# Kernel tuning notes

Hardware: AMD Instinct MI355X
Metric: run time of the kernel (lower is better)

The kernel has to match this reference:

```python
import jax, jax.numpy as jnp
import numpy as np

D, NH, K, FF, S, B = 256, 4, 1024, 1024, 2048, 4  # nhead*d_model must equal key_feature_dim=1024


def _ln(x, g, b, eps=1e-5):
    m = jnp.mean(x, axis=-1, keepdims=True)
    v = jnp.mean((x - m) ** 2, axis=-1, keepdims=True)
    return (x - m) / jnp.sqrt(v + eps) * g + b


def _l2norm(x, eps=1e-12):  # F.normalize(p=2, dim=-1)
    n = jnp.sqrt(jnp.sum(x * x, axis=-1, keepdims=True))
    return x / jnp.maximum(n, eps)


def setup_inputs() -> dict:
    key = jax.random.key(0)
    ks = jax.random.split(key, 16)
    def rn(i, shape, s):
        return jax.random.normal(ks[i], shape, jnp.float32) * jnp.float32(s)
    z = lambda shape: jnp.zeros(shape, jnp.float32)
    o = lambda shape: jnp.ones(shape, jnp.float32)
    return {
        "srcc": jax.random.normal(ks[0], (S, B, D), jnp.float32),
        "memory": jax.random.normal(ks[1], (S, B, D), jnp.float32),
        # per-head RelationUnit weights (stacked over NH heads)
        "WK": rn(2, (NH, K, D), np.sqrt(2.0 / K)),
        "WQ": rn(3, (NH, K, D), np.sqrt(2.0 / K)),
        "WV": rn(4, (NH, D, D), np.sqrt(2.0 / D)),
        "Wt": rn(5, (NH, D, D), np.sqrt(1.0 / D)),   # trans_conv
        # per-head TransNonlinear (extra_nonlinear)
        "e1w": rn(6, (NH, K, D), np.sqrt(1.0 / D)), "e1b": z((NH, K)),
        "e2w": rn(7, (NH, D, K), np.sqrt(1.0 / K)), "e2b": z((NH, D)),
        "eg": o((NH, D)), "eb": z((NH, D)),
        "Wout": rn(8, (D, NH * D), np.sqrt(1.0 / (NH * D))),  # trans_conv_out
        # decoder-layer FFN + norms
        "l1w": rn(9, (FF, D), np.sqrt(1.0 / D)), "l1b": z((FF,)),
        "l2w": rn(10, (D, FF), np.sqrt(1.0 / FF)), "l2b": z((D,)),
        "n1g": o((D,)), "n1b": z((D,)),
        "n3g": o((D,)), "n3b": z((D,)),
    }


def _forward(srcc, memory, WK, WQ, WV, Wt, e1w, e1b, e2w, e2b, eg, eb,
             Wout, l1w, l1b, l2w, l2b, n1g, n1b, n3g, n3b):
    # RMA(query=memory, key=srcc, value=srcc); dropout = identity (eval mode)
    q, kv = memory, srcc  # [S,B,D]
    wk = _l2norm(jnp.einsum('sbd,hkd->hsbk', kv, WK))   # [h,S,B,K]
    wq = _l2norm(jnp.einsum('sbd,hkd->hsbk', q, WQ))
    dot = jnp.einsum('hqbk,hsbk->hbqs', wq, wk)          # [h,B,Sq,Sk]
    aff = jax.nn.softmax(dot, axis=-1)
    # custom renormalization over the *query* axis (torch dim=1 of [B,Sq,Sk])
    aff = aff / (1e-9 + jnp.sum(aff, axis=2, keepdims=True))
    wv = jnp.einsum('sbd,hed->hbse', kv, WV)             # [h,B,Sk,D]
    o = jnp.einsum('hbqs,hbse->hqbe', aff, wv)           # [h,Sq,B,D]
    ru = jax.nn.relu(jnp.einsum('hqbd,hed->hqbe', q[None] - o, Wt))
    # per-head TransNonlinear
    hmid = jax.nn.relu(jnp.einsum('hqbd,hkd->hqbk', ru, e1w) + e1b[:, None, None, :])
    s2 = jnp.einsum('hqbk,hdk->hqbd', hmid, e2w) + e2b[:, None, None, :]
    xh = _ln(ru + s2, eg[:, None, None, :], eb[:, None, None, :])  # [h,S,B,D]
    cat = jnp.moveaxis(xh, 0, 2).reshape(q.shape[0], q.shape[1], NH * D)  # concat heads
    rma_out = jnp.einsum('sbk,dk->sbd', cat, Wout)       # [S,B,D]
    # decoder layer: note the faithful `[0]` indexing from the source
    srcc2 = rma_out[0]                                    # [B,D]
    x = _ln(memory + srcc2[None, :, :], n1g, n1b)         # broadcast residual
    ff = jax.nn.relu(x @ l1w.T + l1b) @ l2w.T + l2b
    return _ln(x + ff, n3g, n3b)


def reference(srcc, memory, WK, WQ, WV, Wt, e1w, e1b, e2w, e2b, eg, eb,
              Wout, l1w, l1b, l2w, l2b, n1g, n1b, n3g, n3b):
    return _forward(srcc, memory, WK, WQ, WV, Wt, e1w, e1b, e2w, e2b, eg, eb,
                    Wout, l1w, l1b, l2w, l2b, n1g, n1b, n3g, n3b)
```

## Files before the change

kernel.cpp:

```cpp
#include <hip/hip_runtime.h>
#include <stdint.h>
#include <stdio.h>

#define S_  2048
#define B_  4
#define D_  256
#define NH_ 4
#define K_  1024
#define FF_ 1024
#define M_  (S_*B_)
#define HB_ (NH_*B_)
#define HBH_ (HB_/2)

#define LDSROW 136

typedef float  f32x4  __attribute__((ext_vector_type(4)));
typedef __bf16 bf16x8 __attribute__((ext_vector_type(8)));

__device__ __forceinline__ float bf2f(unsigned short u) {
  union { unsigned int i; float f; } v; v.i = ((unsigned int)u) << 16; return v.f;
}
__device__ __forceinline__ unsigned short f2bf(float f) {
  union { float f; unsigned int i; } v; v.f = f;
  unsigned int r = v.i + 0x7fffu + ((v.i >> 16) & 1u);
  return (unsigned short)(r >> 16);
}

__device__ __forceinline__ void gld_lds16(const void* g, void* l) {
  __builtin_amdgcn_global_load_lds(
      (__attribute__((address_space(1))) void*)(uintptr_t)g,
      (__attribute__((address_space(3))) void*)(uintptr_t)l, 16, 0, 0);
}

__device__ __forceinline__ void gemm_kloop(
    const unsigned short* __restrict__ Ag, const unsigned short* __restrict__ Bg,
    int lda, int ldb, int kdim,
    unsigned short* __restrict__ smA, unsigned short* __restrict__ smB,
    f32x4 acc[4][4])
{
  const int t    = threadIdx.x;
  const int wave = t >> 6;
  const int lane = t & 63;
  const int wm   = (wave >> 1) << 6;
  const int wn   = (wave & 1) << 6;
  const int c16  = lane & 15;
  const int quad = lane >> 4;

  for (int kc = 0; kc < kdim; kc += 64) {
    __syncthreads();
#pragma unroll
    for (int it = 0; it < 4; ++it) {
      int c   = it*256 + t;
      int row = c >> 3;
      int g   = (c & 7) ^ (row & 7);
      const unsigned short* ga = Ag + (size_t)row*lda + kc + g*8;
      const unsigned short* gb = Bg + (size_t)row*ldb + kc + g*8;
      unsigned short* la = smA + (size_t)(it*256 + wave*64)*8;
      unsigned short* lb = smB + (size_t)(it*256 + wave*64)*8;
      gld_lds16(ga, la);
      gld_lds16(gb, lb);
    }
    asm volatile("s_waitcnt vmcnt(0)" ::: "memory");
    __syncthreads();
#pragma unroll
    for (int ks = 0; ks < 2; ++ks) {
      bf16x8 av[4], bv[4];
#pragma unroll
      for (int i = 0; i < 4; ++i) {
        int ra = wm + i*16 + c16;
        av[i] = *(const bf16x8*)(smA + ra*64 + (((ks*4 + quad) ^ (ra & 7)))*8);
        int rb = wn + i*16 + c16;
        bv[i] = *(const bf16x8*)(smB + rb*64 + (((ks*4 + quad) ^ (rb & 7)))*8);
      }
#pragma unroll
      for (int i = 0; i < 4; ++i)
#pragma unroll
        for (int j = 0; j < 4; ++j)
          acc[i][j] = __builtin_amdgcn_mfma_f32_16x16x32_bf16(av[i], bv[j], acc[i][j], 0, 0, 0);
    }
  }
}

__device__ __forceinline__ float blk_sum256(float v, float* red) {
#pragma unroll
  for (int o = 32; o; o >>= 1) v += __shfl_xor(v, o, 64);
  __syncthreads();
  if ((threadIdx.x & 63) == 0) red[threadIdx.x >> 6] = v;
  __syncthreads();
  return red[0] + red[1] + red[2] + red[3];
}

__global__ void __launch_bounds__(256) k_cvt6(
    const float* __restrict__ s0, unsigned short* __restrict__ d0,
    const float* __restrict__ s1, unsigned short* __restrict__ d1,
    const float* __restrict__ s2, unsigned short* __restrict__ d2,
    const float* __restrict__ s3, unsigned short* __restrict__ d3,
    const float* __restrict__ s4, unsigned short* __restrict__ d4,
    const float* __restrict__ s5, unsigned short* __restrict__ d5) {
  int b = blockIdx.x;
  const float* src; unsigned short* dst; int base;
  if      (b < 2048) { src = s0; dst = d0; base = b; }
  else if (b < 4096) { src = s1; dst = d1; base = b - 2048; }
  else if (b < 5120) { src = s2; dst = d2; base = b - 4096; }
  else if (b < 6144) { src = s3; dst = d3; base = b - 5120; }
  else if (b < 6400) { src = s4; dst = d4; base = b - 6144; }
  else               { src = s5; dst = d5; base = b - 6400; }
  int i = (base*256 + threadIdx.x)*4;
  float4 v = *(const float4*)(src + i);
  ushort4 o;
  o.x = f2bf(v.x); o.y = f2bf(v.y); o.z = f2bf(v.z); o.w = f2bf(v.w);
  *(ushort4*)(dst + i) = o;
}

__global__ void __launch_bounds__(256) k_proj(const unsigned short* __restrict__ X,
    const unsigned short* __restrict__ W, float* __restrict__ nsq,
    unsigned short* __restrict__ outp) {
  __shared__ __align__(16) unsigned short sm[128*LDSROW];
  int l = blockIdx.x, x = l & 7, rblk = l >> 3;
  int m0 = (rblk >> 2)*128;
  int n0 = (x*4 + (rblk & 3))*128;
  f32x4 acc[4][4];
#pragma unroll
  for (int i = 0; i < 4; ++i)
#pragma unroll
    for (int j = 0; j < 4; ++j) acc[i][j] = f32x4{0.f,0.f,0.f,0.f};
  gemm_kloop(X + (size_t)m0*D_, W + (size_t)n0*D_, D_, D_, D_, sm, sm + 128*64, acc);
  const int t = threadIdx.x, wave = t>>6, lane = t&63;
  const int wm = (wave>>1)*64, wn = (wave&1)*64, quad = lane>>4, c16 = lane&15;
  const int h = n0 >> 10;
  __syncthreads();
#pragma unroll
  for (int i = 0; i < 4; ++i)
#pragma unroll
    for (int r = 0; r < 4; ++r) {
      int mloc = wm + i*16 + quad*4 + r;
      float sq = 0.f;
#pragma unroll
      for (int j = 0; j < 4; ++j) {
        float v = acc[i][j][r];
        sm[mloc*LDSROW + wn + j*16 + c16] = f2bf(v);
        sq += v*v;
      }
      sq += __shfl_xor(sq, 1, 64); sq += __shfl_xor(sq, 2, 64);
      sq += __shfl_xor(sq, 4, 64); sq += __shfl_xor(sq, 8, 64);
      if (c16 == 0) {
        int m = m0 + mloc;
        atomicAdd(&nsq[(size_t)(h*B_ + (m & 3))*S_ + (m >> 2)], sq);
      }
    }
  __syncthreads();
  const int col8 = (t & 15)*8, rsub = t >> 4;
#pragma unroll
  for (int c = 0; c < 8; ++c) {
    int mloc = c*16 + rsub;
    int m = m0 + mloc, s = m >> 2, b = m & 3;
    uint4 val = *(const uint4*)(sm + mloc*LDSROW + col8);
    *(uint4*)(outp + ((size_t)(h*B_ + b)*S_ + s)*K_ + (n0 & (K_-1)) + col8) = val;
  }
}

template<int STORE_E>
__global__ void __launch_bounds__(256) k_qkA(const unsigned short* __restrict__ wqa,
    const unsigned short* __restrict__ wka, const float* __restrict__ nq,
    const float* __restrict__ nk, float* __restrict__ lrow,
    unsigned short* __restrict__ E, int hb_base) {
  __shared__ __align__(16) unsigned short sm[128*LDSROW];
  int l = blockIdx.x, x = l & 7, rblk = l >> 3;
  int hb_loc = rblk >> 5;
  int hb = hb_base + hb_loc;
  int rr = rblk & 31;
  int q0 = (x*2 + (rr & 1))*128;
  int s0 = (rr >> 1)*128;
  const unsigned short* A  = wqa + (size_t)hb*S_*K_ + (size_t)q0*K_;
  const unsigned short* Bm = wka + (size_t)hb*S_*K_ + (size_t)s0*K_;
  f32x4 acc[4][4];
#pragma unroll
  for (int i = 0; i < 4; ++i)
#pragma unroll
    for (int j = 0; j < 4; ++j) acc[i][j] = f32x4{0.f,0.f,0.f,0.f};
  gemm_kloop(A, Bm, K_, K_, K_, sm, sm + 128*64, acc);
  const int t = threadIdx.x, wave = t>>6, lane = t&63;
  const int wm = (wave>>1)*64, wn = (wave&1)*64, quad = lane>>4, c16 = lane&15;
  float rk4[4];
#pragma unroll
  for (int j = 0; j < 4; ++j)
    rk4[j] = rsqrtf(nk[(size_t)hb*S_ + s0 + wn + j*16 + c16]);
  __syncthreads();
#pragma unroll
  for (int i = 0; i < 4; ++i)
#pragma unroll
    for (int r = 0; r < 4; ++r) {
      int qloc = wm + i*16 + quad*4 + r;
      float rq = rsqrtf(nq[(size_t)hb*S_ + q0 + qloc]);
      float rs = 0.f;
#pragma unroll
      for (int j = 0; j < 4; ++j) {
        float e = __expf(acc[i][j][r] * rq * rk4[j]);
        rs += e;
        if (STORE_E) sm[qloc*LDSROW + wn + j*16 + c16] = f2bf(e);
      }
      rs += __shfl_xor(rs, 1, 64); rs += __shfl_xor(rs, 2, 64);
      rs += __shfl_xor(rs, 4, 64); rs += __shfl_xor(rs, 8, 64);
      if (c16 == 0) atomicAdd(&lrow[(size_t)hb*S_ + q0 + qloc], rs);
    }
  if (STORE_E) {
    __syncthreads();
    const int col8 = (t & 15)*8, rsub = t >> 4;
#pragma unroll
    for (int c = 0; c < 8; ++c) {
      int qloc = c*16 + rsub;
      uint4 val = *(const uint4*)(sm + qloc*LDSROW + col8);
      *(uint4*)(E + ((size_t)hb_loc*S_ + q0 + qloc)*S_ + s0 + col8) = val;
    }
  }
}

__global__ void __launch_bounds__(256) k_qkB(const unsigned short* __restrict__ wqa,
    const unsigned short* __restrict__ wka, const float* __restrict__ nq,
    const float* __restrict__ nk, const float* __restrict__ lrow,
    float* __restrict__ colsum, float* __restrict__ p0) {
  __shared__ __align__(16) unsigned short smA[128*64], smB[128*64];
  int hb = blockIdx.z;
  int q0 = blockIdx.y*128, s0 = blockIdx.x*128;
  const unsigned short* A  = wqa + (size_t)hb*S_*K_ + (size_t)q0*K_;
  const unsigned short* Bm = wka + (size_t)hb*S_*K_ + (size_t)s0*K_;
  f32x4 acc[4][4];
#pragma unroll
  for (int i = 0; i < 4; ++i)
#pragma unroll
    for (int j = 0; j < 4; ++j) acc[i][j] = f32x4{0.f,0.f,0.f,0.f};
  gemm_kloop(A, Bm, K_, K_, K_, smA, smB, acc);
  const int t = threadIdx.x, wave = t>>6, lane = t&63;
  const int wm = (wave>>1)*64, wn = (wave&1)*64, quad = lane>>4, c16 = lane&15;
  float rk4[4]; int scol[4]; float colp[4] = {0.f,0.f,0.f,0.f};
#pragma unroll
  for (int j = 0; j < 4; ++j) {
    scol[j] = s0 + wn + j*16 + c16;
    rk4[j]  = rsqrtf(nk[(size_t)hb*S_ + scol[j]]);
  }
#pragma unroll
  for (int i = 0; i < 4; ++i)
#pragma unroll
    for (int r = 0; r < 4; ++r) {
      int q = q0 + wm + i*16 + quad*4 + r;
      float rq = rsqrtf(nq[(size_t)hb*S_ + q]);
      float il = 1.f / lrow[(size_t)hb*S_ + q];
#pragma unroll
      for (int j = 0; j < 4; ++j) {
        float p = __expf(acc[i][j][r] * rq * rk4[j]) * il;
        colp[j] += p;
        if (q == 0) p0[(size_t)hb*S_ + scol[j]] = p;
      }
    }
#pragma unroll
  for (int j = 0; j < 4; ++j) {
    float cp = colp[j];
    cp += __shfl_xor(cp, 16, 64); cp += __shfl_xor(cp, 32, 64);
    if (quad == 0) atomicAdd(&colsum[(size_t)hb*S_ + scol[j]], cp);
  }
}

__global__ void __launch_bounds__(256) k_colsumE(const unsigned short* __restrict__ E,
    const float* __restrict__ lrow, float* __restrict__ colsum,
    float* __restrict__ p0, int hb_base) {
  __shared__ float il[128];
  int hb_loc = blockIdx.x, qc = blockIdx.y;
  int hb = hb_base + hb_loc;
  int t  = threadIdx.x;
  if (t < 128) il[t] = 1.f / lrow[(size_t)hb*S_ + qc*128 + t];
  __syncthreads();
  const unsigned short* Eb = E + (size_t)hb_loc*S_*S_ + (size_t)(qc*128)*S_ + t*8;
  float acc8[8] = {0,0,0,0,0,0,0,0};
  for (int qi = 0; qi < 128; ++qi) {
    uint4 u = *(const uint4*)(Eb + (size_t)qi*S_);
    float w = il[qi];
    unsigned int ws_[4] = {u.x, u.y, u.z, u.w};
    float v8[8];
#pragma unroll
    for (int k = 0; k < 4; ++k) {
      v8[2*k]   = bf2f((unsigned short)(ws_[k] & 0xffffu));
      v8[2*k+1] = bf2f((unsigned short)(ws_[k] >> 16));
    }
#pragma unroll
    for (int k = 0; k < 8; ++k) acc8[k] += v8[k] * w;
    if (qc == 0 && qi == 0) {
#pragma unroll
      for (int k = 0; k < 8; ++k) p0[(size_t)hb*S_ + t*8 + k] = v8[k] * w;
    }
  }
#pragma unroll
  for (int k = 0; k < 8; ++k)
    atomicAdd(&colsum[(size_t)hb*S_ + t*8 + k], acc8[k]);
}

__global__ void __launch_bounds__(256) k_mid0(const float* __restrict__ p0,
    const float* __restrict__ colsum, const float* __restrict__ kv,
    float* __restrict__ cbuf) {
  __shared__ float aff[128];
  int hb = blockIdx.x, sc = blockIdx.y;
  int b = hb & 3;
  int t = threadIdx.x;
  if (t < 128) {
    int s = sc*128 + t;
    aff[t] = p0[(size_t)hb*S_ + s] / (1e-9f + colsum[(size_t)hb*S_ + s]);
  }
  __syncthreads();
  float acc = 0.f;
#pragma unroll 4
  for (int i = 0; i < 128; ++i) {
    int s = sc*128 + i;
    acc += aff[i] * kv[((size_t)s*B_ + b)*D_ + t];
  }
  atomicAdd(&cbuf[hb*D_ + t], acc);
}

__global__ void __launch_bounds__(256) k_mid1a(const float* __restrict__ cbuf,
    const float* __restrict__ mem, const float* __restrict__ WV,
    const float* __restrict__ Wt, float* __restrict__ ruW) {
  __shared__ float cS[D_], qmo[D_];
  int hb = blockIdx.x, h = hb >> 2, b = hb & 3;
  int t = threadIdx.x;
  cS[t] = cbuf[hb*D_ + t];
  __syncthreads();
  {
    float a = 0.f;
    const float* row = WV + ((size_t)h*D_ + t)*D_;
#pragma unroll 8
    for (int d = 0; d < D_; ++d) a += cS[d] * row[d];
    qmo[t] = mem[(size_t)b*D_ + t] - a;
  }
  __syncthreads();
  {
    float a = 0.f;
    const float* row = Wt + ((size_t)h*D_ + t)*D_;
#pragma unroll 8
    for (int d = 0; d < D_; ++d) a += qmo[d] * row[d];
    ruW[hb*D_ + t] = fmaxf(a, 0.f);
  }
}

__global__ void __launch_bounds__(256) k_mid1b(const float* __restrict__ ruW,
    const float* __restrict__ e1w, const float* __restrict__ e1b,
    float* __restrict__ hmW) {
  __shared__ float ru[D_];
  int hb = blockIdx.x, kc = blockIdx.y, h = hb >> 2;
  int t = threadIdx.x;
  ru[t] = ruW[hb*D_ + t];
  __syncthreads();
  int k = kc*128 + (t >> 1);
  int half = t & 1;
  const float* row = e1w + ((size_t)h*K_ + k)*D_ + half*128;
  float a = 0.f;
#pragma unroll 8
  for (int d = 0; d < 128; ++d) a += ru[half*128 + d] * row[d];
  a += __shfl_xor(a, 1, 64);
  if (half == 0) hmW[hb*K_ + k] = fmaxf(a + e1b[(size_t)h*K_ + k], 0.f);
}

__global__ void __launch_bounds__(256) k_mid1c(const float* __restrict__ hmW,
    const float* __restrict__ e2w, const float* __restrict__ e2b,
    float* __restrict__ s2W) {
  __shared__ float hm[K_];
  int hb = blockIdx.x, dc = blockIdx.y, h = hb >> 2;
  int t = threadIdx.x;
  for (int k = t; k < K_; k += 256) hm[k] = hmW[hb*K_ + k];
  __syncthreads();
  int d = dc*64 + (t >> 2);
  int part = t & 3;
  const float* row = e2w + ((size_t)h*D_ + d)*K_ + part*256;
  float a = 0.f;
#pragma unroll 8
  for (int k = 0; k < 256; ++k) a += hm[part*256 + k] * row[k];
  a += __shfl_xor(a, 1, 64);
  a += __shfl_xor(a, 2, 64);
  if (part == 0) s2W[hb*D_ + d] = a + e2b[(size_t)h*D_ + d];
}

__global__ void __launch_bounds__(256) k_mid1d(const float* __restrict__ ruW,
    const float* __restrict__ s2W, const float* __restrict__ eg,
    const float* __restrict__ ebias, float* __restrict__ xh0) {
  __shared__ float red[4];
  int hb = blockIdx.x, h = hb >> 2;
  int t = threadIdx.x;
  float tv = ruW[hb*D_ + t] + s2W[hb*D_ + t];
  float mean = blk_sum256(tv, red) * (1.f/D_);
  float dv = tv - mean;
  float var = blk_sum256(dv*dv, red) * (1.f/D_);
  xh0[hb*D_ + t] = dv * rsqrtf(var + 1e-5f) * eg[(size_t)h*D_ + t] + ebias[(size_t)h*D_ + t];
}

__global__ void __launch_bounds__(256) k_mid2(const float* __restrict__ xh0,
    const float* __restrict__ Wout, float* __restrict__ srcc2) {
  __shared__ float cat[NH_*D_];
  int b = blockIdx.x, dc = blockIdx.y, t = threadIdx.x;
  for (int n = t; n < NH_*D_; n += 256)
    cat[n] = xh0[((size_t)(n >> 8)*B_ + b)*D_ + (n & 255)];
  __syncthreads();
  int d = dc*32 + (t >> 3);
  int part = t & 7;
  const float* row = Wout + (size_t)d*(NH_*D_) + part*128;
  float a = 0.f;
#pragma unroll 8
  for (int n = 0; n < 128; ++n) a += cat[part*128 + n] * row[n];
  a += __shfl_xor(a, 1, 64);
  a += __shfl_xor(a, 2, 64);
  a += __shfl_xor(a, 4, 64);
  if (part == 0) srcc2[b*D_ + d] = a;
}

__global__ void __launch_bounds__(256) k_f1(const float* __restrict__ mem,
    const float* __restrict__ srcc2, const float* __restrict__ g,
    const float* __restrict__ bb, float* __restrict__ xf,
    unsigned short* __restrict__ xb) {
  __shared__ float red[4];
  int m = blockIdx.x, t = threadIdx.x;
  float v = mem[(size_t)m*D_ + t] + srcc2[(m & 3)*D_ + t];
  float mean = blk_sum256(v, red) * (1.f/D_);
  float d = v - mean;
  float var = blk_sum256(d*d, red) * (1.f/D_);
  float y = d * rsqrtf(var + 1e-5f) * g[t] + bb[t];
  xf[(size_t)m*D_ + t] = y;
  xb[(size_t)m*D_ + t] = f2bf(y);
}

__global__ void __launch_bounds__(256) k_f2(const unsigned short* __restrict__ xb,
    const unsigned short* __restrict__ l1wb, const float* __restrict__ l1b,
    unsigned short* __restrict__ h1) {
  __shared__ __align__(16) unsigned short sm[128*LDSROW];
  int l = blockIdx.x;
  int n0 = (l & 7)*128, m0 = (l >> 3)*128;
  f32x4 acc[4][4];
#pragma unroll
  for (int i = 0; i < 4; ++i)
#pragma unroll
    for (int j = 0; j < 4; ++j) acc[i][j] = f32x4{0.f,0.f,0.f,0.f};
  gemm_kloop(xb + (size_t)m0*D_, l1wb + (size_t)n0*D_, D_, D_, D_, sm, sm + 128*64, acc);
  const int t = threadIdx.x, wave = t>>6, lane = t&63;
  const int wm = (wave>>1)*64, wn = (wave&1)*64, quad = lane>>4, c16 = lane&15;
  __syncthreads();
#pragma unroll
  for (int i = 0; i < 4; ++i)
#pragma unroll
    for (int r = 0; r < 4; ++r) {
      int mloc = wm + i*16 + quad*4 + r;
#pragma unroll
      for (int j = 0; j < 4; ++j) {
        int n = n0 + wn + j*16 + c16;
        sm[mloc*LDSROW + wn + j*16 + c16] = f2bf(fmaxf(acc[i][j][r] + l1b[n], 0.f));
      }
    }
  __syncthreads();
  const int col8 = (t & 15)*8, rsub = t >> 4;
#pragma unroll
  for (int c = 0; c < 8; ++c) {
    int mloc = c*16 + rsub;
    uint4 val = *(const uint4*)(sm + mloc*LDSROW + col8);
    *(uint4*)(h1 + (size_t)(m0 + mloc)*FF_ + n0 + col8) = val;
  }
}

__global__ void __launch_bounds__(256) k_f3(const unsigned short* __restrict__ h1,
    const unsigned short* __restrict__ l2wb, float* __restrict__ yf) {
  __shared__ __align__(16) unsigned short smA[128*64], smB[128*64];
  int l = blockIdx.x;
  int z = l & 1, n0 = ((l >> 1) & 1)*128, m0 = (l >> 2)*128;
  f32x4 acc[4][4];
#pragma unroll
  for (int i = 0; i < 4; ++i)
#pragma unroll
    for (int j = 0; j < 4; ++j) acc[i][j] = f32x4{0.f,0.f,0.f,0.f};
  gemm_kloop(h1 + (size_t)m0*FF_ + z*512, l2wb + (size_t)n0*FF_ + z*512,
             FF_, FF_, 512, smA, smB, acc);
  const int t = threadIdx.x, wave = t>>6, lane = t&63;
  const int wm = (wave>>1)*64, wn = (wave&1)*64, quad = lane>>4, c16 = lane&15;
#pragma unroll
  for (int i = 0; i < 4; ++i)
#pragma unroll
    for (int r = 0; r < 4; ++r) {
      int m = m0 + wm + i*16 + quad*4 + r;
#pragma unroll
      for (int j = 0; j < 4; ++j) {
        int n = n0 + wn + j*16 + c16;
        atomicAdd(&yf[(size_t)m*D_ + n], acc[i][j][r]);
      }
    }
}

__global__ void __launch_bounds__(256) k_f4(const float* __restrict__ yf,
    const float* __restrict__ l2b, const float* __restrict__ xf,
    const float* __restrict__ g, const float* __restrict__ bb,
    float* __restrict__ out) {
  __shared__ float red[4];
  int m = blockIdx.x, t = threadIdx.x;
  float v = yf[(size_t)m*D_ + t] + l2b[t] + xf[(size_t)m*D_ + t];
  float mean = blk_sum256(v, red) * (1.f/D_);
  float d = v - mean;
  float var = blk_sum256(d*d, red) * (1.f/D_);
  out[(size_t)m*D_ + t] = d * rsqrtf(var + 1e-5f) * g[t] + bb[t];
}

constexpr size_t SZ_ACT  = (size_t)HB_*S_*K_*2;
constexpr size_t SZ_EH   = (size_t)HBH_*S_*S_*2;
constexpr size_t OFF_WQA = 0;
constexpr size_t OFF_WKA = OFF_WQA + SZ_ACT;
constexpr size_t OFF_KVB = OFF_WKA + SZ_ACT;
constexpr size_t OFF_QB  = OFF_KVB + (size_t)M_*D_*2;
constexpr size_t OFF_WKW = OFF_QB  + (size_t)M_*D_*2;
constexpr size_t OFF_WQW = OFF_WKW + (size_t)NH_*K_*D_*2;
constexpr size_t OFF_L1W = OFF_WQW + (size_t)NH_*K_*D_*2;
constexpr size_t OFF_L2W = OFF_L1W + (size_t)FF_*D_*2;
constexpr size_t OFF_XB  = OFF_L2W + (size_t)D_*FF_*2;
constexpr size_t OFF_H1  = OFF_XB  + (size_t)M_*D_*2;
constexpr size_t OFF_XF  = OFF_H1  + (size_t)M_*FF_*2;
constexpr size_t OFF_YF  = OFF_XF  + (size_t)M_*D_*4;
constexpr size_t OFF_NQ  = OFF_YF  + (size_t)M_*D_*4;
constexpr size_t OFF_NK  = OFF_NQ + (size_t)HB_*S_*4;
constexpr size_t OFF_L   = OFF_NK + (size_t)HB_*S_*4;
constexpr size_t OFF_CS  = OFF_L  + (size_t)HB_*S_*4;
constexpr size_t OFF_CB  = OFF_CS + (size_t)HB_*S_*4;
constexpr size_t ZERO_BYTES = (size_t)HB_*S_*4*4 + (size_t)HB_*D_*4;
constexpr size_t OFF_P0  = OFF_CB + (size_t)HB_*D_*4;
constexpr size_t OFF_XH0 = OFF_P0 + (size_t)HB_*S_*4;
constexpr size_t OFF_SC2 = OFF_XH0 + (size_t)HB_*D_*4;
constexpr size_t OFF_RU  = OFF_SC2 + (size_t)B_*D_*4;
constexpr size_t OFF_HM  = OFF_RU  + (size_t)HB_*D_*4;
constexpr size_t OFF_S2  = OFF_HM  + (size_t)HB_*K_*4;
constexpr size_t OFF_E   = OFF_S2  + (size_t)HB_*D_*4;
constexpr size_t NEED_MIN  = OFF_E;
constexpr size_t NEED_FULL = OFF_E + SZ_EH;

extern "C" void kernel_launch(void* const* d_in, const int* in_sizes, int n_in,
                              void* d_out, int out_size, void* d_ws, size_t ws_size,
                              hipStream_t stream) {
  (void)in_sizes; (void)out_size;
  if (n_in < 21) return;
  const float* srcc = (const float*)d_in[0];
  const float* mem  = (const float*)d_in[1];
  const float* WK   = (const float*)d_in[2];
  const float* WQ   = (const float*)d_in[3];
  const float* WV   = (const float*)d_in[4];
  const float* Wt   = (const float*)d_in[5];
  const float* e1w  = (const float*)d_in[6];
  const float* e1b  = (const float*)d_in[7];
  const float* e2w  = (const float*)d_in[8];
  const float* e2b  = (const float*)d_in[9];
  const float* eg   = (const float*)d_in[10];
  const float* eb   = (const float*)d_in[11];
  const float* Wout = (const float*)d_in[12];
  const float* l1w  = (const float*)d_in[13];
  const float* l1b  = (const float*)d_in[14];
  const float* l2w  = (const float*)d_in[15];
  const float* l2b  = (const float*)d_in[16];
  const float* n1g  = (const float*)d_in[17];
  const float* n1b  = (const float*)d_in[18];
  const float* n3g  = (const float*)d_in[19];
  const float* n3b  = (const float*)d_in[20];

  char* ws = (char*)d_ws;
  if (ws_size < NEED_MIN) {
    fprintf(stderr, "kernel_launch: ws_size=%zu < required %zu bytes — aborting\n",
            ws_size, NEED_MIN);
    return;
  }
  const bool useE = (ws_size >= NEED_FULL);

  unsigned short* wqa  = (unsigned short*)(ws + OFF_WQA);
  unsigned short* wka  = (unsigned short*)(ws + OFF_WKA);
  unsigned short* kvb  = (unsigned short*)(ws + OFF_KVB);
  unsigned short* qb   = (unsigned short*)(ws + OFF_QB);
  unsigned short* wkw  = (unsigned short*)(ws + OFF_WKW);
  unsigned short* wqw  = (unsigned short*)(ws + OFF_WQW);
  unsigned short* l1wb = (unsigned short*)(ws + OFF_L1W);
  unsigned short* l2wb = (unsigned short*)(ws + OFF_L2W);
  unsigned short* xb   = (unsigned short*)(ws + OFF_XB);
  unsigned short* h1   = (unsigned short*)(ws + OFF_H1);
  float* xf    = (float*)(ws + OFF_XF);
  float* yf    = (float*)(ws + OFF_YF);
  float* nq    = (float*)(ws + OFF_NQ);
  float* nk    = (float*)(ws + OFF_NK);
  float* lrow  = (float*)(ws + OFF_L);
  float* cs    = (float*)(ws + OFF_CS);
  float* cbuf  = (float*)(ws + OFF_CB);
  float* p0    = (float*)(ws + OFF_P0);
  float* xh0   = (float*)(ws + OFF_XH0);
  float* sc2   = (float*)(ws + OFF_SC2);
  float* ruW   = (float*)(ws + OFF_RU);
  float* hmW   = (float*)(ws + OFF_HM);
  float* s2W   = (float*)(ws + OFF_S2);
  unsigned short* E = (unsigned short*)(ws + OFF_E);

  hipMemsetAsync(ws + OFF_NQ, 0, ZERO_BYTES, stream);
  hipMemsetAsync(ws + OFF_YF, 0, (size_t)M_*D_*4, stream);

  k_cvt6<<<6656, 256, 0, stream>>>(srcc, kvb, mem, qb, WK, wkw, WQ, wqw,
                                   l1w, l1wb, l2w, l2wb);

  k_proj<<<2048, 256, 0, stream>>>(kvb, wkw, nk, wka);
  k_proj<<<2048, 256, 0, stream>>>(qb,  wqw, nq, wqa);

  if (useE) {
    k_qkA<1><<<2048, 256, 0, stream>>>(wqa, wka, nq, nk, lrow, E, 0);
    k_colsumE<<<dim3(HBH_, 16), 256, 0, stream>>>(E, lrow, cs, p0, 0);
    k_qkA<1><<<2048, 256, 0, stream>>>(wqa, wka, nq, nk, lrow, E, HBH_);
    k_colsumE<<<dim3(HBH_, 16), 256, 0, stream>>>(E, lrow, cs, p0, HBH_);
  } else {
    k_qkA<0><<<2048, 256, 0, stream>>>(wqa, wka, nq, nk, lrow, E, 0);
    k_qkA<0><<<2048, 256, 0, stream>>>(wqa, wka, nq, nk, lrow, E, HBH_);
    dim3 gq(S_/128, S_/128, HB_);
    k_qkB<<<gq, 256, 0, stream>>>(wqa, wka, nq, nk, lrow, cs, p0);
  }

  k_mid0<<<dim3(HB_, S_/128), 256, 0, stream>>>(p0, cs, srcc, cbuf);
  k_mid1a<<<HB_, 256, 0, stream>>>(cbuf, mem, WV, Wt, ruW);
  k_mid1b<<<dim3(HB_, 8), 256, 0, stream>>>(ruW, e1w, e1b, hmW);
  k_mid1c<<<dim3(HB_, 4), 256, 0, stream>>>(hmW, e2w, e2b, s2W);
  k_mid1d<<<HB_, 256, 0, stream>>>(ruW, s2W, eg, eb, xh0);
  k_mid2<<<dim3(B_, 8), 256, 0, stream>>>(xh0, Wout, sc2);

  k_f1<<<M_, 256, 0, stream>>>(mem, sc2, n1g, n1b, xf, xb);
  k_f2<<<512, 256, 0, stream>>>(xb, l1wb, l1b, h1);
  k_f3<<<256, 256, 0, stream>>>(h1, l2wb, yf);
  k_f4<<<M_, 256, 0, stream>>>(yf, l2b, xf, n3g, n3b, (float*)d_out);
}
```

Before: 681.8 us.

## Store normalized projections in fp8 and use fp8 MFMA for QK affinity

Projection outputs for query and key features are now written as fp8 instead of bf16, and the QK affinity GEMM uses fp8 MFMA with a new 128-byte-chunk LDS staging loop. This halves activation traffic and doubles nominal MFMA throughput. The E buffer now covers all head-batches in one launch, removing the half-split path and the recompute fallback. The small mid-stage matvec kernels are rewritten to wave-per-row float4 reductions with fewer blocks. Fp8 quantization of the projections risks accuracy loss in the cosine-similarity softmax.

```diff
diff --git a/kernel.cpp b/kernel.cpp
--- a/kernel.cpp
+++ b/kernel.cpp
@@ -10,9 +10,9 @@
 #define FF_ 1024
 #define M_  (S_*B_)
 #define HB_ (NH_*B_)
-#define HBH_ (HB_/2)
 
 #define LDSROW 136
+#define PROW 144
 
 typedef float  f32x4  __attribute__((ext_vector_type(4)));
 typedef __bf16 bf16x8 __attribute__((ext_vector_type(8)));
@@ -24,6 +24,9 @@
   union { float f; unsigned int i; } v; v.f = f;
   unsigned int r = v.i + 0x7fffu + ((v.i >> 16) & 1u);
   return (unsigned short)(r >> 16);
+}
+__device__ __forceinline__ unsigned char f2fp8(float f) {
+  return (unsigned char)(__builtin_amdgcn_cvt_pk_fp8_f32(f, f, 0, false) & 0xff);
 }
 
 __device__ __forceinline__ void gld_lds16(const void* g, void* l) {
@@ -88,6 +91,12 @@
   if ((threadIdx.x & 63) == 0) red[threadIdx.x >> 6] = v;
   __syncthreads();
   return red[0] + red[1] + red[2] + red[3];
+}
+
+__device__ __forceinline__ float wave_red(float a) {
+#pragma unroll
+  for (int o = 1; o < 64; o <<= 1) a += __shfl_xor(a, o, 64);
+  return a;
 }
 
 __global__ void __launch_bounds__(256) k_cvt6(
@@ -114,7 +123,7 @@
 
 __global__ void __launch_bounds__(256) k_proj(const unsigned short* __restrict__ X,
     const unsigned short* __restrict__ W, float* __restrict__ nsq,
-    unsigned short* __restrict__ outp) {
+    unsigned char* __restrict__ outp) {
   __shared__ __align__(16) unsigned short sm[128*LDSROW];
   int l = blockIdx.x, x = l & 7, rblk = l >> 3;
   int m0 = (rblk >> 2)*128;
@@ -128,6 +137,7 @@
   const int t = threadIdx.x, wave = t>>6, lane = t&63;
   const int wm = (wave>>1)*64, wn = (wave&1)*64, quad = lane>>4, c16 = lane&15;
   const int h = n0 >> 10;
+  unsigned char* sm8 = (unsigned char*)sm;
   __syncthreads();
 #pragma unroll
   for (int i = 0; i < 4; ++i)
@@ -138,7 +148,7 @@
 #pragma unroll
       for (int j = 0; j < 4; ++j) {
         float v = acc[i][j][r];
-        sm[mloc*LDSROW + wn + j*16 + c16] = f2bf(v);
+        sm8[mloc*PROW + wn + j*16 + c16] = f2fp8(v);
         sq += v*v;
       }
       sq += __shfl_xor(sq, 1, 64); sq += __shfl_xor(sq, 2, 64);
@@ -149,38 +159,68 @@
       }
     }
   __syncthreads();
-  const int col8 = (t & 15)*8, rsub = t >> 4;
-#pragma unroll
-  for (int c = 0; c < 8; ++c) {
-    int mloc = c*16 + rsub;
+  const int cg = t & 7, rsub = t >> 3;
+#pragma unroll
+  for (int c = 0; c < 4; ++c) {
+    int mloc = c*32 + rsub;
     int m = m0 + mloc, s = m >> 2, b = m & 3;
-    uint4 val = *(const uint4*)(sm + mloc*LDSROW + col8);
-    *(uint4*)(outp + ((size_t)(h*B_ + b)*S_ + s)*K_ + (n0 & (K_-1)) + col8) = val;
-  }
-}
-
-template<int STORE_E>
-__global__ void __launch_bounds__(256) k_qkA(const unsigned short* __restrict__ wqa,
-    const unsigned short* __restrict__ wka, const float* __restrict__ nq,
+    uint4 val = *(const uint4*)(sm8 + mloc*PROW + cg*16);
+    *(uint4*)(outp + ((size_t)(h*B_ + b)*S_ + s)*K_ + (n0 & (K_-1)) + cg*16) = val;
+  }
+}
+
+__global__ void __launch_bounds__(256) k_qkA(const unsigned char* __restrict__ wqa,
+    const unsigned char* __restrict__ wka, const float* __restrict__ nq,
     const float* __restrict__ nk, float* __restrict__ lrow,
-    unsigned short* __restrict__ E, int hb_base) {
+    unsigned short* __restrict__ E) {
   __shared__ __align__(16) unsigned short sm[128*LDSROW];
+  unsigned char* smA = (unsigned char*)sm;
+  unsigned char* smB = smA + 128*128;
   int l = blockIdx.x, x = l & 7, rblk = l >> 3;
-  int hb_loc = rblk >> 5;
-  int hb = hb_base + hb_loc;
+  int hb = rblk >> 5;
   int rr = rblk & 31;
   int q0 = (x*2 + (rr & 1))*128;
   int s0 = (rr >> 1)*128;
-  const unsigned short* A  = wqa + (size_t)hb*S_*K_ + (size_t)q0*K_;
-  const unsigned short* Bm = wka + (size_t)hb*S_*K_ + (size_t)s0*K_;
-  f32x4 acc[4][4];
-#pragma unroll
-  for (int i = 0; i < 4; ++i)
-#pragma unroll
-    for (int j = 0; j < 4; ++j) acc[i][j] = f32x4{0.f,0.f,0.f,0.f};
-  gemm_kloop(A, Bm, K_, K_, K_, sm, sm + 128*64, acc);
+  const unsigned char* A  = wqa + (size_t)hb*S_*K_ + (size_t)q0*K_;
+  const unsigned char* Bm = wka + (size_t)hb*S_*K_ + (size_t)s0*K_;
   const int t = threadIdx.x, wave = t>>6, lane = t&63;
   const int wm = (wave>>1)*64, wn = (wave&1)*64, quad = lane>>4, c16 = lane&15;
+  f32x4 acc[4][4];
+#pragma unroll
+  for (int i = 0; i < 4; ++i)
+#pragma unroll
+    for (int j = 0; j < 4; ++j) acc[i][j] = f32x4{0.f,0.f,0.f,0.f};
+
+  for (int kc = 0; kc < K_; kc += 128) {
+    __syncthreads();
+#pragma unroll
+    for (int it = 0; it < 4; ++it) {
+      int c   = it*256 + t;
+      int row = c >> 3;
+      int g   = (c & 7) ^ (row & 7);
+      gld_lds16(A  + (size_t)row*K_ + kc + g*16, smA + (size_t)(it*256 + wave*64)*16);
+      gld_lds16(Bm + (size_t)row*K_ + kc + g*16, smB + (size_t)(it*256 + wave*64)*16);
+    }
+    asm volatile("s_waitcnt vmcnt(0)" ::: "memory");
+    __syncthreads();
+#pragma unroll
+    for (int ks = 0; ks < 4; ++ks) {
+      long av[4], bv[4];
+#pragma unroll
+      for (int i = 0; i < 4; ++i) {
+        int ra = wm + i*16 + c16;
+        av[i] = *(const long*)(smA + ra*128 + (((2*ks + (quad>>1)) ^ (ra & 7)))*16 + (quad&1)*8);
+        int rb = wn + i*16 + c16;
+        bv[i] = *(const long*)(smB + rb*128 + (((2*ks + (quad>>1)) ^ (rb & 7)))*16 + (quad&1)*8);
+      }
+#pragma unroll
+      for (int i = 0; i < 4; ++i)
+#pragma unroll
+        for (int j = 0; j < 4; ++j)
+          acc[i][j] = __builtin_amdgcn_mfma_f32_16x16x32_fp8_fp8(av[i], bv[j], acc[i][j], 0, 0, 0);
+    }
+  }
+
   float rk4[4];
 #pragma unroll
   for (int j = 0; j < 4; ++j)
@@ -197,79 +237,31 @@
       for (int j = 0; j < 4; ++j) {
         float e = __expf(acc[i][j][r] * rq * rk4[j]);
         rs += e;
-        if (STORE_E) sm[qloc*LDSROW + wn + j*16 + c16] = f2bf(e);
+        sm[qloc*LDSROW + wn + j*16 + c16] = f2bf(e);
       }
       rs += __shfl_xor(rs, 1, 64); rs += __shfl_xor(rs, 2, 64);
       rs += __shfl_xor(rs, 4, 64); rs += __shfl_xor(rs, 8, 64);
       if (c16 == 0) atomicAdd(&lrow[(size_t)hb*S_ + q0 + qloc], rs);
     }
-  if (STORE_E) {
-    __syncthreads();
-    const int col8 = (t & 15)*8, rsub = t >> 4;
-#pragma unroll
-    for (int c = 0; c < 8; ++c) {
-      int qloc = c*16 + rsub;
-      uint4 val = *(const uint4*)(sm + qloc*LDSROW + col8);
-      *(uint4*)(E + ((size_t)hb_loc*S_ + q0 + qloc)*S_ + s0 + col8) = val;
-    }
-  }
-}
-
-__global__ void __launch_bounds__(256) k_qkB(const unsigned short* __restrict__ wqa,
-    const unsigned short* __restrict__ wka, const float* __restrict__ nq,
-    const float* __restrict__ nk, const float* __restrict__ lrow,
-    float* __restrict__ colsum, float* __restrict__ p0) {
-  __shared__ __align__(16) unsigned short smA[128*64], smB[128*64];
-  int hb = blockIdx.z;
-  int q0 = blockIdx.y*128, s0 = blockIdx.x*128;
-  const unsigned short* A  = wqa + (size_t)hb*S_*K_ + (size_t)q0*K_;
-  const unsigned short* Bm = wka + (size_t)hb*S_*K_ + (size_t)s0*K_;
-  f32x4 acc[4][4];
-#pragma unroll
-  for (int i = 0; i < 4; ++i)
-#pragma unroll
-    for (int j = 0; j < 4; ++j) acc[i][j] = f32x4{0.f,0.f,0.f,0.f};
-  gemm_kloop(A, Bm, K_, K_, K_, smA, smB, acc);
-  const int t = threadIdx.x, wave = t>>6, lane = t&63;
-  const int wm = (wave>>1)*64, wn = (wave&1)*64, quad = lane>>4, c16 = lane&15;
-  float rk4[4]; int scol[4]; float colp[4] = {0.f,0.f,0.f,0.f};
-#pragma unroll
-  for (int j = 0; j < 4; ++j) {
-    scol[j] = s0 + wn + j*16 + c16;
-    rk4[j]  = rsqrtf(nk[(size_t)hb*S_ + scol[j]]);
-  }
-#pragma unroll
-  for (int i = 0; i < 4; ++i)
-#pragma unroll
-    for (int r = 0; r < 4; ++r) {
-      int q = q0 + wm + i*16 + quad*4 + r;
-      float rq = rsqrtf(nq[(size_t)hb*S_ + q]);
-      float il = 1.f / lrow[(size_t)hb*S_ + q];
-#pragma unroll
-      for (int j = 0; j < 4; ++j) {
-        float p = __expf(acc[i][j][r] * rq * rk4[j]) * il;
-        colp[j] += p;
-        if (q == 0) p0[(size_t)hb*S_ + scol[j]] = p;
-      }
-    }
-#pragma unroll
-  for (int j = 0; j < 4; ++j) {
-    float cp = colp[j];
-    cp += __shfl_xor(cp, 16, 64); cp += __shfl_xor(cp, 32, 64);
-    if (quad == 0) atomicAdd(&colsum[(size_t)hb*S_ + scol[j]], cp);
+  __syncthreads();
+  const int col8 = (t & 15)*8, rsub = t >> 4;
+#pragma unroll
+  for (int c = 0; c < 8; ++c) {
+    int qloc = c*16 + rsub;
+    uint4 val = *(const uint4*)(sm + qloc*LDSROW + col8);
+    *(uint4*)(E + ((size_t)hb*S_ + q0 + qloc)*S_ + s0 + col8) = val;
   }
 }
 
 __global__ void __launch_bounds__(256) k_colsumE(const unsigned short* __restrict__ E,
     const float* __restrict__ lrow, float* __restrict__ colsum,
-    float* __restrict__ p0, int hb_base) {
+    float* __restrict__ p0) {
   __shared__ float il[128];
-  int hb_loc = blockIdx.x, qc = blockIdx.y;
-  int hb = hb_base + hb_loc;
+  int hb = blockIdx.x, qc = blockIdx.y;
   int t  = threadIdx.x;
   if (t < 128) il[t] = 1.f / lrow[(size_t)hb*S_ + qc*128 + t];
   __syncthreads();
-  const unsigned short* Eb = E + (size_t)hb_loc*S_*S_ + (size_t)(qc*128)*S_ + t*8;
+  const unsigned short* Eb = E + (size_t)hb*S_*S_ + (size_t)(qc*128)*S_ + t*8;
   float acc8[8] = {0,0,0,0,0,0,0,0};
   for (int qi = 0; qi < 128; ++qi) {
     uint4 u = *(const uint4*)(Eb + (size_t)qi*S_);
@@ -319,23 +311,23 @@
     const float* __restrict__ Wt, float* __restrict__ ruW) {
   __shared__ float cS[D_], qmo[D_];
   int hb = blockIdx.x, h = hb >> 2, b = hb & 3;
-  int t = threadIdx.x;
+  int t = threadIdx.x, wave = t >> 6, lane = t & 63;
   cS[t] = cbuf[hb*D_ + t];
   __syncthreads();
-  {
-    float a = 0.f;
-    const float* row = WV + ((size_t)h*D_ + t)*D_;
-#pragma unroll 8
-    for (int d = 0; d < D_; ++d) a += cS[d] * row[d];
-    qmo[t] = mem[(size_t)b*D_ + t] - a;
-  }
-  __syncthreads();
-  {
-    float a = 0.f;
-    const float* row = Wt + ((size_t)h*D_ + t)*D_;
-#pragma unroll 8
-    for (int d = 0; d < D_; ++d) a += qmo[d] * row[d];
-    ruW[hb*D_ + t] = fmaxf(a, 0.f);
+  float4 cv = *(const float4*)(cS + lane*4);
+  for (int rr = 0; rr < 64; ++rr) {
+    int e = wave*64 + rr;
+    float4 w = *(const float4*)(WV + ((size_t)h*D_ + e)*D_ + lane*4);
+    float a = wave_red(cv.x*w.x + cv.y*w.y + cv.z*w.z + cv.w*w.w);
+    if (lane == 0) qmo[e] = mem[(size_t)b*D_ + e] - a;
+  }
+  __syncthreads();
+  float4 qv = *(const float4*)(qmo + lane*4);
+  for (int rr = 0; rr < 64; ++rr) {
+    int e = wave*64 + rr;
+    float4 w = *(const float4*)(Wt + ((size_t)h*D_ + e)*D_ + lane*4);
+    float a = wave_red(qv.x*w.x + qv.y*w.y + qv.z*w.z + qv.w*w.w);
+    if (lane == 0) ruW[hb*D_ + e] = fmaxf(a, 0.f);
   }
 }
 
@@ -344,17 +336,16 @@
     float* __restrict__ hmW) {
   __shared__ float ru[D_];
   int hb = blockIdx.x, kc = blockIdx.y, h = hb >> 2;
-  int t = threadIdx.x;
+  int t = threadIdx.x, wave = t >> 6, lane = t & 63;
   ru[t] = ruW[hb*D_ + t];
   __syncthreads();
-  int k = kc*128 + (t >> 1);
-  int half = t & 1;
-  const float* row = e1w + ((size_t)h*K_ + k)*D_ + half*128;
-  float a = 0.f;
-#pragma unroll 8
-  for (int d = 0; d < 128; ++d) a += ru[half*128 + d] * row[d];
-  a += __shfl_xor(a, 1, 64);
-  if (half == 0) hmW[hb*K_ + k] = fmaxf(a + e1b[(size_t)h*K_ + k], 0.f);
+  float4 rv = *(const float4*)(ru + lane*4);
+  for (int rr = 0; rr < 32; ++rr) {
+    int k = kc*128 + wave*32 + rr;
+    float4 w = *(const float4*)(e1w + ((size_t)h*K_ + k)*D_ + lane*4);
+    float a = wave_red(rv.x*w.x + rv.y*w.y + rv.z*w.z + rv.w*w.w);
+    if (lane == 0) hmW[hb*K_ + k] = fmaxf(a + e1b[(size_t)h*K_ + k], 0.f);
+  }
 }
 
 __global__ void __launch_bounds__(256) k_mid1c(const float* __restrict__ hmW,
@@ -362,18 +353,22 @@
     float* __restrict__ s2W) {
   __shared__ float hm[K_];
   int hb = blockIdx.x, dc = blockIdx.y, h = hb >> 2;
-  int t = threadIdx.x;
+  int t = threadIdx.x, wave = t >> 6, lane = t & 63;
   for (int k = t; k < K_; k += 256) hm[k] = hmW[hb*K_ + k];
   __syncthreads();
-  int d = dc*64 + (t >> 2);
-  int part = t & 3;
-  const float* row = e2w + ((size_t)h*D_ + d)*K_ + part*256;
-  float a = 0.f;
-#pragma unroll 8
-  for (int k = 0; k < 256; ++k) a += hm[part*256 + k] * row[k];
-  a += __shfl_xor(a, 1, 64);
-  a += __shfl_xor(a, 2, 64);
-  if (part == 0) s2W[hb*D_ + d] = a + e2b[(size_t)h*D_ + d];
+  for (int rr = 0; rr < 32; ++rr) {
+    int d = dc*128 + wave*32 + rr;
+    const float* row = e2w + ((size_t)h*D_ + d)*K_;
+    float a = 0.f;
+#pragma unroll
+    for (int p = 0; p < 4; ++p) {
+      float4 w = *(const float4*)(row + (p*64 + lane)*4);
+      float4 hv = *(const float4*)(hm + (p*64 + lane)*4);
+      a += w.x*hv.x + w.y*hv.y + w.z*hv.z + w.w*hv.w;
+    }
+    a = wave_red(a);
+    if (lane == 0) s2W[hb*D_ + d] = a + e2b[(size_t)h*D_ + d];
+  }
 }
 
 __global__ void __launch_bounds__(256) k_mid1d(const float* __restrict__ ruW,
@@ -392,20 +387,24 @@
 __global__ void __launch_bounds__(256) k_mid2(const float* __restrict__ xh0,
     const float* __restrict__ Wout, float* __restrict__ srcc2) {
   __shared__ float cat[NH_*D_];
-  int b = blockIdx.x, dc = blockIdx.y, t = threadIdx.x;
+  int b = blockIdx.x, dc = blockIdx.y;
+  int t = threadIdx.x, wave = t >> 6, lane = t & 63;
   for (int n = t; n < NH_*D_; n += 256)
     cat[n] = xh0[((size_t)(n >> 8)*B_ + b)*D_ + (n & 255)];
   __syncthreads();
-  int d = dc*32 + (t >> 3);
-  int part = t & 7;
-  const float* row = Wout + (size_t)d*(NH_*D_) + part*128;
-  float a = 0.f;
-#pragma unroll 8
-  for (int n = 0; n < 128; ++n) a += cat[part*128 + n] * row[n];
-  a += __shfl_xor(a, 1, 64);
-  a += __shfl_xor(a, 2, 64);
-  a += __shfl_xor(a, 4, 64);
-  if (part == 0) srcc2[b*D_ + d] = a;
+  for (int rr = 0; rr < 32; ++rr) {
+    int d = dc*128 + wave*32 + rr;
+    const float* row = Wout + (size_t)d*(NH_*D_);
+    float a = 0.f;
+#pragma unroll
+    for (int p = 0; p < 4; ++p) {
+      float4 w = *(const float4*)(row + (p*64 + lane)*4);
+      float4 cv = *(const float4*)(cat + (p*64 + lane)*4);
+      a += w.x*cv.x + w.y*cv.y + w.z*cv.z + w.w*cv.w;
+    }
+    a = wave_red(a);
+    if (lane == 0) srcc2[b*D_ + d] = a;
+  }
 }
 
 __global__ void __launch_bounds__(256) k_f1(const float* __restrict__ mem,
@@ -499,8 +498,7 @@
   out[(size_t)m*D_ + t] = d * rsqrtf(var + 1e-5f) * g[t] + bb[t];
 }
 
-constexpr size_t SZ_ACT  = (size_t)HB_*S_*K_*2;
-constexpr size_t SZ_EH   = (size_t)HBH_*S_*S_*2;
+constexpr size_t SZ_ACT  = (size_t)HB_*S_*K_;
 constexpr size_t OFF_WQA = 0;
 constexpr size_t OFF_WKA = OFF_WQA + SZ_ACT;
 constexpr size_t OFF_KVB = OFF_WKA + SZ_ACT;
@@ -526,8 +524,8 @@
 constexpr size_t OFF_HM  = OFF_RU  + (size_t)HB_*D_*4;
 constexpr size_t OFF_S2  = OFF_HM  + (size_t)HB_*K_*4;
 constexpr size_t OFF_E   = OFF_S2  + (size_t)HB_*D_*4;
-constexpr size_t NEED_MIN  = OFF_E;
-constexpr size_t NEED_FULL = OFF_E + SZ_EH;
+constexpr size_t SZ_E    = (size_t)HB_*S_*S_*2;
+constexpr size_t NEED_ALL = OFF_E + SZ_E;
 
 extern "C" void kernel_launch(void* const* d_in, const int* in_sizes, int n_in,
                               void* d_out, int out_size, void* d_ws, size_t ws_size,
@@ -557,15 +555,14 @@
   const float* n3b  = (const float*)d_in[20];
 
   char* ws = (char*)d_ws;
-  if (ws_size < NEED_MIN) {
+  if (ws_size < NEED_ALL) {
     fprintf(stderr, "kernel_launch: ws_size=%zu < required %zu bytes — aborting\n",
-            ws_size, NEED_MIN);
+            ws_size, NEED_ALL);
     return;
   }
-  const bool useE = (ws_size >= NEED_FULL);
-
-  unsigned short* wqa  = (unsigned short*)(ws + OFF_WQA);
-  unsigned short* wka  = (unsigned short*)(ws + OFF_WKA);
+
+  unsigned char*  wqa  = (unsigned char*)(ws + OFF_WQA);
+  unsigned char*  wka  = (unsigned char*)(ws + OFF_WKA);
   unsigned short* kvb  = (unsigned short*)(ws + OFF_KVB);
   unsigned short* qb   = (unsigned short*)(ws + OFF_QB);
   unsigned short* wkw  = (unsigned short*)(ws + OFF_WKW);
@@ -598,24 +595,15 @@
   k_proj<<<2048, 256, 0, stream>>>(kvb, wkw, nk, wka);
   k_proj<<<2048, 256, 0, stream>>>(qb,  wqw, nq, wqa);
 
-  if (useE) {
-    k_qkA<1><<<2048, 256, 0, stream>>>(wqa, wka, nq, nk, lrow, E, 0);
-    k_colsumE<<<dim3(HBH_, 16), 256, 0, stream>>>(E, lrow, cs, p0, 0);
-    k_qkA<1><<<2048, 256, 0, stream>>>(wqa, wka, nq, nk, lrow, E, HBH_);
-    k_colsumE<<<dim3(HBH_, 16), 256, 0, stream>>>(E, lrow, cs, p0, HBH_);
-  } else {
-    k_qkA<0><<<2048, 256, 0, stream>>>(wqa, wka, nq, nk, lrow, E, 0);
-    k_qkA<0><<<2048, 256, 0, stream>>>(wqa, wka, nq, nk, lrow, E, HBH_);
-    dim3 gq(S_/128, S_/128, HB_);
-    k_qkB<<<gq, 256, 0, stream>>>(wqa, wka, nq, nk, lrow, cs, p0);
-  }
+  k_qkA<<<4096, 256, 0, stream>>>(wqa, wka, nq, nk, lrow, E);
+  k_colsumE<<<dim3(HB_, 16), 256, 0, stream>>>(E, lrow, cs, p0);
 
   k_mid0<<<dim3(HB_, S_/128), 256, 0, stream>>>(p0, cs, srcc, cbuf);
   k_mid1a<<<HB_, 256, 0, stream>>>(cbuf, mem, WV, Wt, ruW);
   k_mid1b<<<dim3(HB_, 8), 256, 0, stream>>>(ruW, e1w, e1b, hmW);
-  k_mid1c<<<dim3(HB_, 4), 256, 0, stream>>>(hmW, e2w, e2b, s2W);
+  k_mid1c<<<dim3(HB_, 2), 256, 0, stream>>>(hmW, e2w, e2b, s2W);
   k_mid1d<<<HB_, 256, 0, stream>>>(ruW, s2W, eg, eb, xh0);
-  k_mid2<<<dim3(B_, 8), 256, 0, stream>>>(xh0, Wout, sc2);
+  k_mid2<<<dim3(B_, 2), 256, 0, stream>>>(xh0, Wout, sc2);
 
   k_f1<<<M_, 256, 0, stream>>>(mem, sc2, n1g, n1b, xf, xb);
   k_f2<<<512, 256, 0, stream>>>(xb, l1wb, l1b, h1);
```

Result: slower. 700.1 us (+2.7%).
